# Kernel tuning notes

Hardware: AMD Instinct MI355X
Metric: run time of the kernel (lower is better)

The kernel has to match this reference:

```python
import jax, jax.numpy as jnp
import numpy as np

NEG_SLOPE = 0.2


def gat_layer(x_src, x_dst, src, dst, W, a_src, a_dst, b, n_dst, H, C):
    # Linear transform: [Ns, H, C] / [Nd, H, C]
    h_s = (x_src @ W).reshape(-1, H, C)
    h_d = (x_dst @ W).reshape(-1, H, C)
    # Per-edge attention logits: a . [x_i || x_j] (x_i = dst/target, x_j = src)
    e = jnp.einsum('ehc,hc->eh', h_s[src], a_src) + jnp.einsum('ehc,hc->eh', h_d[dst], a_dst)
    e = jax.nn.leaky_relu(e, NEG_SLOPE)  # [E, H]
    # Segment softmax over destination neighborhoods
    m = jax.ops.segment_max(e, dst, num_segments=n_dst)          # [Nd, H]
    ex = jnp.exp(e - m[dst])
    denom = jax.ops.segment_sum(ex, dst, num_segments=n_dst)    # [Nd, H]
    alpha = ex / denom[dst]                                      # [E, H]
    # Weighted scatter-sum aggregation
    out = jax.ops.segment_sum(alpha[:, :, None] * h_s[src], dst, num_segments=n_dst)
    return out.reshape(n_dst, H * C) + b


def setup_inputs() -> dict:
    key = jax.random.key(0)
    ks = jax.random.split(key, 16)
    N, F_IN, OUT = 200000, 602, 41
    N1, N1D, E1 = 120000, 30000, 960000
    N2D, E2 = 6000, 192000
    s = 0.05
    return {
        'x': jax.random.normal(ks[0], (N, F_IN), jnp.float32),
        'n_id1': jax.random.randint(ks[1], (N1,), 0, N),
        'res_n_id1': jax.random.randint(ks[2], (N1D,), 0, N1),
        'edge_src1': jax.random.randint(ks[3], (E1,), 0, N1),
        'edge_dst1': jax.random.randint(ks[4], (E1,), 0, N1D),
        'res_n_id2': jax.random.randint(ks[5], (N2D,), 0, N1D),
        'edge_src2': jax.random.randint(ks[6], (E2,), 0, N1D),
        'edge_dst2': jax.random.randint(ks[7], (E2,), 0, N2D),
        'W1': jax.random.normal(ks[8], (F_IN, 64), jnp.float32) * s,
        'att_src1': jax.random.normal(ks[9], (8, 8), jnp.float32) * s,
        'att_dst1': jax.random.normal(ks[10], (8, 8), jnp.float32) * s,
        'bias1': jax.random.normal(ks[11], (64,), jnp.float32) * s,
        'W2': jax.random.normal(ks[12], (64, OUT), jnp.float32) * s,
        'att_src2': jax.random.normal(ks[13], (1, OUT), jnp.float32) * s,
        'att_dst2': jax.random.normal(ks[14], (1, OUT), jnp.float32) * s,
        'bias2': jax.random.normal(ks[15], (OUT,), jnp.float32) * s,
    }


def reference(x, n_id1, res_n_id1, edge_src1, edge_dst1, res_n_id2, edge_src2,
              edge_dst2, W1, att_src1, att_dst1, bias1, W2, att_src2, att_dst2, bias2):
    # Block 1: gather frontier, GATConv(in -> 8, heads=8, concat) -> [N1D, 64]
    h = x[n_id1]
    h = gat_layer(h, h[res_n_id1], edge_src1, edge_dst1,
                  W1, att_src1, att_dst1, bias1, res_n_id1.shape[0], 8, 8)
    h = jax.nn.elu(h)
    # (dropout p=0.6 is identity in eval mode)
    # Block 2: GATConv(64 -> out, heads=1) -> [N2D, out]
    h = gat_layer(h, h[res_n_id2], edge_src2, edge_dst2,
                  W2, att_src2, att_dst2, bias2, res_n_id2.shape[0], 1, W2.shape[1])
    return jax.nn.log_softmax(h, axis=1)
```

## Files before the change

kernel.cpp:

```cpp
#include <hip/hip_runtime.h>
#include <hip/hip_bf16.h>
#include <math.h>

typedef __attribute__((ext_vector_type(8))) short short8;
typedef __attribute__((ext_vector_type(4))) float float4v;

__device__ __forceinline__ float wave_max64(float v) {
#pragma unroll
  for (int o = 32; o > 0; o >>= 1) v = fmaxf(v, __shfl_xor(v, o));
  return v;
}
__device__ __forceinline__ float wave_sum64(float v) {
#pragma unroll
  for (int o = 32; o > 0; o >>= 1) v += __shfl_xor(v, o);
  return v;
}
__device__ __forceinline__ float lrelu02(float v) { return v > 0.f ? v : 0.2f * v; }
__device__ __forceinline__ short bf16_rne(float f) {
  unsigned u = __builtin_bit_cast(unsigned, f);
  unsigned r = (u + 0x7FFFu + ((u >> 16) & 1u)) >> 16;
  return (short)r;
}

__global__ void hist_prepack_kernel(const int* __restrict__ dst1, const int* __restrict__ dst2,
                                    int* __restrict__ counts, const float* __restrict__ W,
                                    short* __restrict__ Wp, int E1, int E2, int N1D, int nbE) {
  int b = blockIdx.x;
  if (b < nbE) {
    int e = b * 256 + threadIdx.x;
    if (e < E1) atomicAdd(&counts[dst1[e]], 1);
    else if (e < E1 + E2) atomicAdd(&counts[N1D + dst2[e - E1]], 1);
  } else {
    int idx = (b - nbE) * 256 + threadIdx.x;
    if (idx >= 19 * 4 * 64) return;
    int lane = idx & 63;
    int t = (idx >> 6) & 3;
    int s = idx >> 8;
    int quad = lane >> 4, n = t * 16 + (lane & 15);
    short8 v;
#pragma unroll
    for (int j = 0; j < 8; j++) {
      int k = s * 32 + quad * 8 + j;
      v[j] = (k < 602) ? bf16_rne(W[k * 64 + n]) : (short)0;
    }
    *((short8*)Wp + idx) = v;
  }
}

__global__ __launch_bounds__(256) void scan1_kernel(const int* __restrict__ counts,
                                                    int* __restrict__ offs,
                                                    int* __restrict__ bsum, int n) {
  __shared__ int ws[4], wpre[4];
  int tid = threadIdx.x, lane = tid & 63, w = tid >> 6;
  int i = blockIdx.x * 256 + tid;
  int v = (i < n) ? counts[i] : 0;
  int x = v;
#pragma unroll
  for (int o = 1; o < 64; o <<= 1) {
    int y = __shfl_up(x, o);
    if (lane >= o) x += y;
  }
  if (lane == 63) ws[w] = x;
  __syncthreads();
  if (tid == 0) {
    int run = 0;
#pragma unroll
    for (int k = 0; k < 4; k++) { wpre[k] = run; run += ws[k]; }
    bsum[blockIdx.x] = run;
  }
  __syncthreads();
  if (i < n) offs[i] = x - v + wpre[w];
}

__global__ __launch_bounds__(256) void scan2_kernel(int* __restrict__ bsum, int nb) {
  __shared__ int ws[4], wpre[4];
  int tid = threadIdx.x, lane = tid & 63, w = tid >> 6;
  int v = (tid < nb) ? bsum[tid] : 0;
  int x = v;
#pragma unroll
  for (int o = 1; o < 64; o <<= 1) {
    int y = __shfl_up(x, o);
    if (lane >= o) x += y;
  }
  if (lane == 63) ws[w] = x;
  __syncthreads();
  if (tid == 0) {
    int run = 0;
#pragma unroll
    for (int k = 0; k < 4; k++) { wpre[k] = run; run += ws[k]; }
  }
  __syncthreads();
  if (tid < nb) bsum[tid] = x - v + wpre[w];
}

__global__ __launch_bounds__(256) void scan3_kernel(int* __restrict__ offs,
                                                    const int* __restrict__ bsum,
                                                    int n, int etot) {
  int i = blockIdx.x * 256 + threadIdx.x;
  if (i < n) offs[i] += bsum[blockIdx.x];
  if (i == 0) offs[n] = etot;
}

__global__ __launch_bounds__(256) void gemm1_fused_kernel(
    const float* __restrict__ x, const int* __restrict__ n_id,
    const short* __restrict__ Wp, const float* __restrict__ as1,
    float* __restrict__ out, float* __restrict__ ssrc1, int M, int nbG,
    const int* __restrict__ dst1, const int* __restrict__ src1,
    const int* __restrict__ dst2, const int* __restrict__ src2,
    const int* __restrict__ offs, int* __restrict__ cursor,
    int* __restrict__ epay, int E1, int E2, int N1D) {
  if (blockIdx.x >= nbG) {
    int e = (blockIdx.x - nbG) * 256 + threadIdx.x;
    if (e < E1) {
      int d = dst1[e];
      int pos = offs[d] + atomicAdd(&cursor[d], 1);
      epay[pos] = src1[e];
    } else if (e < E1 + E2) {
      int e2 = e - E1;
      int d = N1D + dst2[e2];
      int pos = offs[d] + atomicAdd(&cursor[d], 1);
      epay[pos] = src2[e2];
    }
    return;
  }
  constexpr int K = 602, NSTEP = 19;
  int tid = threadIdx.x;
  int wid = tid >> 6, lane = tid & 63;
  int quad = lane >> 4, mrow = lane & 15;
  int r = blockIdx.x * 64 + wid * 16 + mrow;
  int grow = n_id[r < M ? r : M - 1];
  const float* xrow = x + (size_t)grow * K;
  float4v acc[4] = {{0.f, 0.f, 0.f, 0.f}, {0.f, 0.f, 0.f, 0.f},
                    {0.f, 0.f, 0.f, 0.f}, {0.f, 0.f, 0.f, 0.f}};
  for (int s = 0; s < NSTEP; s++) {
    int k0 = s * 32 + quad * 8;
    float af[8];
    if (k0 + 8 <= K) {
#pragma unroll
      for (int j = 0; j < 8; j += 2) {
        float2 v = *(const float2*)(xrow + k0 + j);
        af[j] = v.x;
        af[j + 1] = v.y;
      }
    } else {
#pragma unroll
      for (int j = 0; j < 8; j++) af[j] = (k0 + j < K) ? xrow[k0 + j] : 0.f;
    }
    short8 a;
#pragma unroll
    for (int j = 0; j < 8; j++) a[j] = bf16_rne(af[j]);
    const short8* wp = (const short8*)Wp + (size_t)s * 256 + lane;
#pragma unroll
    for (int t = 0; t < 4; t++) {
      short8 b = wp[t * 64];
      acc[t] = __builtin_amdgcn_mfma_f32_16x16x32_bf16(a, b, acc[t], 0, 0, 0);
    }
  }
  int rb = blockIdx.x * 64 + wid * 16;
#pragma unroll
  for (int t = 0; t < 4; t++) {
#pragma unroll
    for (int j = 0; j < 4; j++) {
      int rr = rb + quad * 4 + j;
      if (rr < M) out[(size_t)rr * 64 + t * 16 + mrow] = acc[t][j];
    }
  }
  float afv[4];
#pragma unroll
  for (int t = 0; t < 4; t++) afv[t] = as1[t * 16 + mrow];
#pragma unroll
  for (int t = 0; t < 4; t++) {
#pragma unroll
    for (int j = 0; j < 4; j++) {
      float v = acc[t][j] * afv[t];
      v += __shfl_xor(v, 1);
      v += __shfl_xor(v, 2);
      v += __shfl_xor(v, 4);
      if ((lane & 7) == 0) {
        int rr = rb + quad * 4 + j;
        if (rr < M) ssrc1[rr * 8 + t * 2 + ((lane >> 3) & 1)] = v;
      }
    }
  }
}

__global__ __launch_bounds__(256) void agg1_kernel(
    const int* __restrict__ offs, const int* __restrict__ srcs,
    const float* __restrict__ s_src, const int* __restrict__ res,
    const float* __restrict__ ad, const float* __restrict__ hs1,
    const float* __restrict__ bias, const float* __restrict__ W2,
    const float* __restrict__ as2, float* __restrict__ hs2,
    float* __restrict__ ssrc2, int n_dst) {
  constexpr int C = 41;
  __shared__ float Ws[64 * C];
  __shared__ float rowsh[4][64];
  for (int i = threadIdx.x; i < 64 * C; i += 256) Ws[i] = W2[i];
  __syncthreads();
  int wid = (blockIdx.x * blockDim.x + threadIdx.x) >> 6;
  if (wid >= n_dst) return;
  int lane = threadIdx.x & 63;
  int w = threadIdx.x >> 6;
  int h = lane >> 3;
  int node = res[wid];
  float v = hs1[(size_t)node * 64 + lane] * ad[lane];
  v += __shfl_xor(v, 1);
  v += __shfl_xor(v, 2);
  v += __shfl_xor(v, 4);
  float sd = v;
  int beg = offs[wid], end = offs[wid + 1];
  float mx = -1e30f, den = 0.f, acc = 0.f;
  for (int i = beg; i < end; i += 8) {
    int m = end - i; if (m > 8) m = 8;
    int sr[8]; float ss[8], row[8];
#pragma unroll
    for (int j = 0; j < 8; j++) sr[j] = srcs[i + (j < m ? j : 0)];
#pragma unroll
    for (int j = 0; j < 8; j++) ss[j] = s_src[sr[j] * 8 + h];
#pragma unroll
    for (int j = 0; j < 8; j++) row[j] = hs1[(size_t)sr[j] * 64 + lane];
    float p[8];
#pragma unroll
    for (int j = 0; j < 8; j++) p[j] = (j < m) ? lrelu02(ss[j] + sd) : -1e30f;
    float bm = mx;
#pragma unroll
    for (int j = 0; j < 8; j++) bm = fmaxf(bm, p[j]);
    float scale = __expf(mx - bm);
    den *= scale;
    acc *= scale;
#pragma unroll
    for (int j = 0; j < 8; j++) {
      float w2 = __expf(p[j] - bm);
      den += w2;
      acc += w2 * row[j];
    }
    mx = bm;
  }
  float val = (end > beg) ? acc / den : 0.f;
  val += bias[lane];
  val = val > 0.f ? val : __expf(val) - 1.f;
  rowsh[w][lane] = val;
  float acc2 = 0.f;
  if (lane < C) {
#pragma unroll 8
    for (int k = 0; k < 64; k++) acc2 += rowsh[w][k] * Ws[k * C + lane];
  }
  float tt = (lane < C) ? acc2 * as2[lane] : 0.f;
  tt = wave_sum64(tt);
  if (lane == 0) ssrc2[wid] = tt;
  if (lane < C) hs2[(size_t)wid * C + lane] = acc2;
}

__global__ __launch_bounds__(256) void agg2_kernel(
    const int* __restrict__ offs, const int* __restrict__ srcs,
    const float* __restrict__ s_src, const int* __restrict__ res,
    const float* __restrict__ ad, const float* __restrict__ hs2,
    const float* __restrict__ bias, float* __restrict__ out, int n_dst) {
  constexpr int C = 41;
  int wid = (blockIdx.x * blockDim.x + threadIdx.x) >> 6;
  if (wid >= n_dst) return;
  int lane = threadIdx.x & 63;
  bool act = lane < C;
  int node = res[wid];
  float dv = act ? hs2[(size_t)node * C + lane] * ad[lane] : 0.f;
  float sd = wave_sum64(dv);
  int beg = offs[wid], end = offs[wid + 1];
  float mx = -1e30f, den = 0.f, acc = 0.f;
  for (int i = beg; i < end; i += 8) {
    int m = end - i; if (m > 8) m = 8;
    int sr[8]; float ss[8], row[8];
#pragma unroll
    for (int j = 0; j < 8; j++) sr[j] = srcs[i + (j < m ? j : 0)];
#pragma unroll
    for (int j = 0; j < 8; j++) ss[j] = s_src[sr[j]];
#pragma unroll
    for (int j = 0; j < 8; j++) row[j] = act ? hs2[(size_t)sr[j] * C + lane] : 0.f;
    float p[8];
#pragma unroll
    for (int j = 0; j < 8; j++) p[j] = (j < m) ? lrelu02(ss[j] + sd) : -1e30f;
    float bm = mx;
#pragma unroll
    for (int j = 0; j < 8; j++) bm = fmaxf(bm, p[j]);
    float scale = __expf(mx - bm);
    den *= scale;
    acc *= scale;
#pragma unroll
    for (int j = 0; j < 8; j++) {
      float w = __expf(p[j] - bm);
      den += w;
      acc += w * row[j];
    }
    mx = bm;
  }
  float val = (end > beg) ? acc / den : 0.f;
  if (act) val += bias[lane];
  float lv = act ? val : -1e30f;
  float m2 = wave_max64(lv);
  float ex = act ? __expf(val - m2) : 0.f;
  float ssum = wave_sum64(ex);
  if (act) out[(size_t)wid * C + lane] = val - m2 - __logf(ssum);
}

extern "C" void kernel_launch(void* const* d_in, const int* in_sizes, int n_in,
                              void* d_out, int out_size, void* d_ws, size_t ws_size,
                              hipStream_t stream) {
  const float* x    = (const float*)d_in[0];
  const int* n_id1  = (const int*)d_in[1];
  const int* res1   = (const int*)d_in[2];
  const int* esrc1  = (const int*)d_in[3];
  const int* edst1  = (const int*)d_in[4];
  const int* res2   = (const int*)d_in[5];
  const int* esrc2  = (const int*)d_in[6];
  const int* edst2  = (const int*)d_in[7];
  const float* W1   = (const float*)d_in[8];
  const float* as1  = (const float*)d_in[9];
  const float* ad1  = (const float*)d_in[10];
  const float* b1   = (const float*)d_in[11];
  const float* W2   = (const float*)d_in[12];
  const float* as2  = (const float*)d_in[13];
  const float* ad2  = (const float*)d_in[14];
  const float* b2   = (const float*)d_in[15];
  float* out = (float*)d_out;

  const int N1  = in_sizes[1];
  const int N1D = in_sizes[2];
  const int E1  = in_sizes[3];
  const int N2D = in_sizes[5];
  const int E2  = in_sizes[6];
  const int NTOT = N1D + N2D;
  const int ETOT = E1 + E2;

  char* w = (char*)d_ws;
  size_t off = 0;
  auto alloc = [&](size_t bytes) -> void* {
    void* p = (void*)(w + off);
    off += (bytes + 255) & ~(size_t)255;
    return p;
  };
  float* hs1   = (float*)alloc((size_t)N1 * 64 * 4);
  float* ssrc1 = (float*)alloc((size_t)N1 * 8 * 4);
  float* hs2   = (float*)alloc((size_t)N1D * 41 * 4);
  float* ssrc2 = (float*)alloc((size_t)N1D * 4);
  int* counts  = (int*)alloc((size_t)2 * NTOT * 4);
  int* cursor  = counts + NTOT;
  int* offs    = (int*)alloc((size_t)(NTOT + 1) * 4);
  int* bsum    = (int*)alloc((size_t)256 * 4);
  int* epay    = (int*)alloc((size_t)ETOT * 4);
  short* Wp    = (short*)alloc((size_t)19 * 4 * 64 * 8 * 2);
  (void)ws_size; (void)n_in; (void)out_size;

  hipMemsetAsync(counts, 0, (size_t)2 * NTOT * 4, stream);

  const int nbE = (ETOT + 255) / 256;
  const int nb = (NTOT + 255) / 256;
  hist_prepack_kernel<<<nbE + 19, 256, 0, stream>>>(edst1, edst2, counts, W1, Wp, E1, E2, N1D, nbE);
  scan1_kernel<<<nb, 256, 0, stream>>>(counts, offs, bsum, NTOT);
  scan2_kernel<<<1, 256, 0, stream>>>(bsum, nb);
  scan3_kernel<<<nb, 256, 0, stream>>>(offs, bsum, NTOT, ETOT);

  const int nbG = (N1 + 63) / 64;
  gemm1_fused_kernel<<<nbG + nbE, 256, 0, stream>>>(
      x, n_id1, Wp, as1, hs1, ssrc1, N1, nbG,
      edst1, esrc1, edst2, esrc2, offs, cursor, epay, E1, E2, N1D);
  agg1_kernel<<<(N1D + 3) / 4, 256, 0, stream>>>(offs, epay, ssrc1, res1, ad1, hs1, b1,
                                                 W2, as2, hs2, ssrc2, N1D);

  agg2_kernel<<<(N2D + 3) / 4, 256, 0, stream>>>(offs + N1D, epay, ssrc2, res2, ad2, hs2, b2, out, N2D);
}
```

Before: 811.7 us.

## Store hs1 as bf16, record edge ranks in histogram, fold scan2 into scan3

The first-layer transformed features hs1 are now written and read as bf16, which halves the bytes gathered per edge in agg1. The histogram kernel records each edge's atomic rank, so the CSR fill writes directly without a second atomic cursor pass. The separate single-block scan2 is removed, and each scan3 block sums the earlier block totals itself. Edge-fill blocks are placed ahead of the GEMM blocks. The cost is lower precision for hs1, plus an extra rank array that is written and then read back.

```diff
diff --git a/kernel.cpp b/kernel.cpp
--- a/kernel.cpp
+++ b/kernel.cpp
@@ -4,6 +4,7 @@
 
 typedef __attribute__((ext_vector_type(8))) short short8;
 typedef __attribute__((ext_vector_type(4))) float float4v;
+typedef unsigned short ushort_t;
 
 __device__ __forceinline__ float wave_max64(float v) {
 #pragma unroll
@@ -11,6 +12,11 @@
   return v;
 }
 __device__ __forceinline__ float wave_sum64(float v) {
+#pragma unroll
+  for (int o = 32; o > 0; o >>= 1) v += __shfl_xor(v, o);
+  return v;
+}
+__device__ __forceinline__ int wave_isum64(int v) {
 #pragma unroll
   for (int o = 32; o > 0; o >>= 1) v += __shfl_xor(v, o);
   return v;
@@ -21,15 +27,22 @@
   unsigned r = (u + 0x7FFFu + ((u >> 16) & 1u)) >> 16;
   return (short)r;
 }
+__device__ __forceinline__ float bf16_to_f32(ushort_t u) {
+  return __builtin_bit_cast(float, ((unsigned)u) << 16);
+}
 
 __global__ void hist_prepack_kernel(const int* __restrict__ dst1, const int* __restrict__ dst2,
-                                    int* __restrict__ counts, const float* __restrict__ W,
+                                    int* __restrict__ counts, int* __restrict__ erank,
+                                    const float* __restrict__ W,
                                     short* __restrict__ Wp, int E1, int E2, int N1D, int nbE) {
   int b = blockIdx.x;
   if (b < nbE) {
     int e = b * 256 + threadIdx.x;
-    if (e < E1) atomicAdd(&counts[dst1[e]], 1);
-    else if (e < E1 + E2) atomicAdd(&counts[N1D + dst2[e - E1]], 1);
+    if (e < E1) {
+      erank[e] = atomicAdd(&counts[dst1[e]], 1);
+    } else if (e < E1 + E2) {
+      erank[e] = atomicAdd(&counts[N1D + dst2[e - E1]], 1);
+    }
   } else {
     int idx = (b - nbE) * 256 + threadIdx.x;
     if (idx >= 19 * 4 * 64) return;
@@ -72,62 +85,48 @@
   if (i < n) offs[i] = x - v + wpre[w];
 }
 
-__global__ __launch_bounds__(256) void scan2_kernel(int* __restrict__ bsum, int nb) {
-  __shared__ int ws[4], wpre[4];
-  int tid = threadIdx.x, lane = tid & 63, w = tid >> 6;
-  int v = (tid < nb) ? bsum[tid] : 0;
-  int x = v;
-#pragma unroll
-  for (int o = 1; o < 64; o <<= 1) {
-    int y = __shfl_up(x, o);
-    if (lane >= o) x += y;
-  }
-  if (lane == 63) ws[w] = x;
-  __syncthreads();
-  if (tid == 0) {
-    int run = 0;
-#pragma unroll
-    for (int k = 0; k < 4; k++) { wpre[k] = run; run += ws[k]; }
-  }
-  __syncthreads();
-  if (tid < nb) bsum[tid] = x - v + wpre[w];
-}
-
 __global__ __launch_bounds__(256) void scan3_kernel(int* __restrict__ offs,
                                                     const int* __restrict__ bsum,
-                                                    int n, int etot) {
-  int i = blockIdx.x * 256 + threadIdx.x;
-  if (i < n) offs[i] += bsum[blockIdx.x];
+                                                    int n, int etot, int nb) {
+  __shared__ int wsum[4];
+  int tid = threadIdx.x, lane = tid & 63, w = tid >> 6;
+  int bid = blockIdx.x;
+  int v = (tid < nb && tid < bid) ? bsum[tid] : 0;
+  v = wave_isum64(v);
+  if (lane == 0) wsum[w] = v;
+  __syncthreads();
+  int pre = wsum[0] + wsum[1] + wsum[2] + wsum[3];
+  int i = bid * 256 + tid;
+  if (i < n) offs[i] += pre;
   if (i == 0) offs[n] = etot;
 }
 
 __global__ __launch_bounds__(256) void gemm1_fused_kernel(
     const float* __restrict__ x, const int* __restrict__ n_id,
     const short* __restrict__ Wp, const float* __restrict__ as1,
-    float* __restrict__ out, float* __restrict__ ssrc1, int M, int nbG,
+    ushort_t* __restrict__ out, float* __restrict__ ssrc1, int M, int nbE,
     const int* __restrict__ dst1, const int* __restrict__ src1,
     const int* __restrict__ dst2, const int* __restrict__ src2,
-    const int* __restrict__ offs, int* __restrict__ cursor,
+    const int* __restrict__ offs, const int* __restrict__ erank,
     int* __restrict__ epay, int E1, int E2, int N1D) {
-  if (blockIdx.x >= nbG) {
-    int e = (blockIdx.x - nbG) * 256 + threadIdx.x;
+  if (blockIdx.x < nbE) {
+    int e = blockIdx.x * 256 + threadIdx.x;
     if (e < E1) {
       int d = dst1[e];
-      int pos = offs[d] + atomicAdd(&cursor[d], 1);
-      epay[pos] = src1[e];
+      epay[offs[d] + erank[e]] = src1[e];
     } else if (e < E1 + E2) {
       int e2 = e - E1;
       int d = N1D + dst2[e2];
-      int pos = offs[d] + atomicAdd(&cursor[d], 1);
-      epay[pos] = src2[e2];
+      epay[offs[d] + erank[e]] = src2[e2];
     }
     return;
   }
   constexpr int K = 602, NSTEP = 19;
+  int gb = blockIdx.x - nbE;
   int tid = threadIdx.x;
   int wid = tid >> 6, lane = tid & 63;
   int quad = lane >> 4, mrow = lane & 15;
-  int r = blockIdx.x * 64 + wid * 16 + mrow;
+  int r = gb * 64 + wid * 16 + mrow;
   int grow = n_id[r < M ? r : M - 1];
   const float* xrow = x + (size_t)grow * K;
   float4v acc[4] = {{0.f, 0.f, 0.f, 0.f}, {0.f, 0.f, 0.f, 0.f},
@@ -156,13 +155,13 @@
       acc[t] = __builtin_amdgcn_mfma_f32_16x16x32_bf16(a, b, acc[t], 0, 0, 0);
     }
   }
-  int rb = blockIdx.x * 64 + wid * 16;
+  int rb = gb * 64 + wid * 16;
 #pragma unroll
   for (int t = 0; t < 4; t++) {
 #pragma unroll
     for (int j = 0; j < 4; j++) {
       int rr = rb + quad * 4 + j;
-      if (rr < M) out[(size_t)rr * 64 + t * 16 + mrow] = acc[t][j];
+      if (rr < M) out[(size_t)rr * 64 + t * 16 + mrow] = (ushort_t)bf16_rne(acc[t][j]);
     }
   }
   float afv[4];
@@ -187,7 +186,7 @@
 __global__ __launch_bounds__(256) void agg1_kernel(
     const int* __restrict__ offs, const int* __restrict__ srcs,
     const float* __restrict__ s_src, const int* __restrict__ res,
-    const float* __restrict__ ad, const float* __restrict__ hs1,
+    const float* __restrict__ ad, const ushort_t* __restrict__ hs1,
     const float* __restrict__ bias, const float* __restrict__ W2,
     const float* __restrict__ as2, float* __restrict__ hs2,
     float* __restrict__ ssrc2, int n_dst) {
@@ -202,7 +201,7 @@
   int w = threadIdx.x >> 6;
   int h = lane >> 3;
   int node = res[wid];
-  float v = hs1[(size_t)node * 64 + lane] * ad[lane];
+  float v = bf16_to_f32(hs1[(size_t)node * 64 + lane]) * ad[lane];
   v += __shfl_xor(v, 1);
   v += __shfl_xor(v, 2);
   v += __shfl_xor(v, 4);
@@ -217,7 +216,7 @@
 #pragma unroll
     for (int j = 0; j < 8; j++) ss[j] = s_src[sr[j] * 8 + h];
 #pragma unroll
-    for (int j = 0; j < 8; j++) row[j] = hs1[(size_t)sr[j] * 64 + lane];
+    for (int j = 0; j < 8; j++) row[j] = bf16_to_f32(hs1[(size_t)sr[j] * 64 + lane]);
     float p[8];
 #pragma unroll
     for (int j = 0; j < 8; j++) p[j] = (j < m) ? lrelu02(ss[j] + sd) : -1e30f;
@@ -336,31 +335,31 @@
     off += (bytes + 255) & ~(size_t)255;
     return p;
   };
-  float* hs1   = (float*)alloc((size_t)N1 * 64 * 4);
+  ushort_t* hs1 = (ushort_t*)alloc((size_t)N1 * 64 * 2);
   float* ssrc1 = (float*)alloc((size_t)N1 * 8 * 4);
   float* hs2   = (float*)alloc((size_t)N1D * 41 * 4);
   float* ssrc2 = (float*)alloc((size_t)N1D * 4);
-  int* counts  = (int*)alloc((size_t)2 * NTOT * 4);
-  int* cursor  = counts + NTOT;
+  int* counts  = (int*)alloc((size_t)NTOT * 4);
   int* offs    = (int*)alloc((size_t)(NTOT + 1) * 4);
   int* bsum    = (int*)alloc((size_t)256 * 4);
   int* epay    = (int*)alloc((size_t)ETOT * 4);
+  int* erank   = (int*)alloc((size_t)ETOT * 4);
   short* Wp    = (short*)alloc((size_t)19 * 4 * 64 * 8 * 2);
   (void)ws_size; (void)n_in; (void)out_size;
 
-  hipMemsetAsync(counts, 0, (size_t)2 * NTOT * 4, stream);
+  hipMemsetAsync(counts, 0, (size_t)NTOT * 4, stream);
 
   const int nbE = (ETOT + 255) / 256;
   const int nb = (NTOT + 255) / 256;
-  hist_prepack_kernel<<<nbE + 19, 256, 0, stream>>>(edst1, edst2, counts, W1, Wp, E1, E2, N1D, nbE);
+  hist_prepack_kernel<<<nbE + 19, 256, 0, stream>>>(edst1, edst2, counts, erank, W1, Wp,
+                                                    E1, E2, N1D, nbE);
   scan1_kernel<<<nb, 256, 0, stream>>>(counts, offs, bsum, NTOT);
-  scan2_kernel<<<1, 256, 0, stream>>>(bsum, nb);
-  scan3_kernel<<<nb, 256, 0, stream>>>(offs, bsum, NTOT, ETOT);
+  scan3_kernel<<<nb, 256, 0, stream>>>(offs, bsum, NTOT, ETOT, nb);
 
   const int nbG = (N1 + 63) / 64;
-  gemm1_fused_kernel<<<nbG + nbE, 256, 0, stream>>>(
-      x, n_id1, Wp, as1, hs1, ssrc1, N1, nbG,
-      edst1, esrc1, edst2, esrc2, offs, cursor, epay, E1, E2, N1D);
+  gemm1_fused_kernel<<<nbE + nbG, 256, 0, stream>>>(
+      x, n_id1, Wp, as1, hs1, ssrc1, N1, nbE,
+      edst1, esrc1, edst2, esrc2, offs, erank, epay, E1, E2, N1D);
   agg1_kernel<<<(N1D + 3) / 4, 256, 0, stream>>>(offs, epay, ssrc1, res1, ad1, hs1, b1,
                                                  W2, as2, hs2, ssrc2, N1D);
 
```

Result: faster. 785.4 us (-3.2%).
